# Optimization experiments

Measured on AMD Instinct MI355X. Metric: run time of the kernel, lower is better.

Reference implementation:

```python
import jax, jax.numpy as jnp
import numpy as np

# Topologies derived from init kwargs (inputs=64, outputs=64, state=512, net1 hidden=[512])
D = 64 + 64 + 512                      # 640 = concat(input, prev_output, state)
NET1 = [D, 512, 64]
NET3 = [D] + NET1 + [512]              # [640, 640, 512, 64, 512] (code reuses mutated net1 topo)
W_TOTAL = sum(NET3[j] * NET3[j + 1] for j in range(len(NET3) - 1))  # 802816
B_TOTAL = sum(NET3[1:])                # 1728
NET2 = [D] + NET1 + [W_TOTAL + B_TOTAL]  # [640, 640, 512, 64, 804544]


def _leaky(v):
    return jnp.where(v >= 0, v, 0.01 * v)


def setup_inputs() -> dict:
    key = jax.random.key(0)
    ks = jax.random.split(key, 16)
    inp = {
        "x": jax.random.normal(ks[0], (64,), jnp.float32),
        "prev_output": jnp.zeros((64,), jnp.float32),
        "state": jnp.zeros((512,), jnp.float32),
    }
    # net1 params (Linear stores W as [out, in])
    for i in range(len(NET1) - 1):
        inp[f"net1_w{i}"] = jax.random.normal(ks[1 + i], (NET1[i + 1], NET1[i]), jnp.float32) * 0.02
        inp[f"net1_b{i}"] = jnp.zeros((NET1[i + 1],), jnp.float32)
    # net2 params
    for i in range(len(NET2) - 1):
        inp[f"net2_w{i}"] = jax.random.normal(ks[5 + i], (NET2[i + 1], NET2[i]), jnp.float32) * 0.02
        inp[f"net2_b{i}"] = jnp.zeros((NET2[i + 1],), jnp.float32)
    return inp


def reference(x, prev_output, state,
              net1_w0, net1_b0, net1_w1, net1_b1,
              net2_w0, net2_b0, net2_w1, net2_b1,
              net2_w2, net2_b2, net2_w3, net2_b3):
    inpt = jnp.concatenate([x, prev_output, state])  # [640]

    # net2: hypernetwork producing flattened weights+biases for net3
    h = _leaky(net2_w0 @ inpt + net2_b0)
    h = _leaky(net2_w1 @ h + net2_b1)
    h = _leaky(net2_w2 @ h + net2_b2)
    x2 = jnp.tanh(net2_w3 @ h + net2_b3) * 0.5       # [W_TOTAL + B_TOTAL]
    weights = x2[:W_TOTAL]
    bias = x2[W_TOTAL:]

    # net3: apply generated weights sequentially (state update)
    x3 = inpt
    wi, bi = 0, 0
    for j in range(1, len(NET3)):
        out_d, in_d = NET3[j], NET3[j - 1]
        W = weights[wi:wi + out_d * in_d].reshape(out_d, in_d)
        b = bias[bi:bi + out_d]
        x3 = W @ x3 + b                               # 1D: x3 @ W.T == W @ x3
        if j != len(NET3) - 1:
            x3 = _leaky(x3)
        wi += out_d * in_d
        bi += out_d
    new_state = x3                                    # [512]

    # net1: output head
    h1 = _leaky(net1_w0 @ inpt + net1_b0)
    out = net1_w1 @ h1 + net1_b1                      # [64]

    # torch forward returns only `out`; new_state is the persistent buffer
    # update. We concatenate both so the full step math is observable.
    return jnp.concatenate([out, new_state])          # [576]
```

## Files before the change

kernel.cpp:

```cpp
#include <hip/hip_runtime.h>
#include <math.h>


#define WS_H0    0
#define WS_H1N1  640
#define WS_H1N2  1152
#define WS_H2    1664
#define WS_INPT  1728
#define WS_X3A   2368
#define WS_X3B   3008
#define WS_T     4096

#define N_ROWS   804544
#define N_WAVES  12571

typedef float vf4 __attribute__((ext_vector_type(4)));

__device__ __forceinline__ float leaky_f(float v) { return v >= 0.0f ? v : 0.01f * v; }

__device__ __forceinline__ float inpt_at(int i, const float* x, const float* po, const float* st) {
  return i < 64 ? x[i] : (i < 128 ? po[i - 64] : st[i - 128]);
}

__device__ __forceinline__ float half_tanh(float d) {
  float t = exp2f(d * 2.8853900817779268f);
  return 0.5f - __builtin_amdgcn_rcpf(t + 1.0f);
}

template <int IN>
__device__ __forceinline__ float row_dot(const float* __restrict__ wrow, const float* s_in, int lane) {
  const float4* w4 = (const float4*)wrow;
  const float4* s4 = (const float4*)s_in;
  float acc = 0.f;
  for (int j = lane; j < IN / 4; j += 64) {
    float4 a = w4[j];
    float4 b = s4[j];
    acc += a.x * b.x + a.y * b.y + a.z * b.z + a.w * b.w;
  }
  for (int off = 32; off; off >>= 1) acc += __shfl_xor(acc, off, 64);
  return acc;
}

__global__ __launch_bounds__(256) void k1a(const float* __restrict__ x, const float* __restrict__ po,
                                           const float* __restrict__ st,
                                           const float* __restrict__ w2_0, const float* __restrict__ b2_0,
                                           const float* __restrict__ w1_0, const float* __restrict__ b1_0,
                                           float* __restrict__ ws) {
  __shared__ __align__(16) float s_in[640];
  for (int i = threadIdx.x; i < 640; i += 256) {
    float v = inpt_at(i, x, po, st);
    s_in[i] = v;
    ws[WS_INPT + i] = v;
  }
  __syncthreads();
  int wave = threadIdx.x >> 6, lane = threadIdx.x & 63;
  int o = blockIdx.x * 4 + wave;
  const float* wrow;
  float bias;
  float* dst;
  if (o < 640) {
    wrow = w2_0 + (long long)o * 640; bias = b2_0[o]; dst = ws + WS_H0 + o;
  } else {
    int oo = o - 640;
    wrow = w1_0 + (long long)oo * 640; bias = b1_0[oo]; dst = ws + WS_H1N1 + oo;
  }
  float acc = row_dot<640>(wrow, s_in, lane);
  if (lane == 0) *dst = leaky_f(acc + bias);
}

__global__ __launch_bounds__(256) void k1b(const float* __restrict__ w2_1, const float* __restrict__ b2_1,
                                           const float* __restrict__ w1_1, const float* __restrict__ b1_1,
                                           float* __restrict__ ws, float* __restrict__ out) {
  __shared__ __align__(16) float s_h0[640];
  __shared__ __align__(16) float s_h1[512];
  for (int i = threadIdx.x; i < 640; i += 256) s_h0[i] = ws[WS_H0 + i];
  for (int i = threadIdx.x; i < 512; i += 256) s_h1[i] = ws[WS_H1N1 + i];
  __syncthreads();
  int wave = threadIdx.x >> 6, lane = threadIdx.x & 63;
  int o = blockIdx.x * 4 + wave;
  if (o < 512) {
    float acc = row_dot<640>(w2_1 + (long long)o * 640, s_h0, lane);
    if (lane == 0) ws[WS_H1N2 + o] = leaky_f(acc + b2_1[o]);
  } else {
    int oo = o - 512;
    float acc = row_dot<512>(w1_1 + (long long)oo * 512, s_h1, lane);
    if (lane == 0) out[oo] = acc + b1_1[oo];
  }
}

__global__ __launch_bounds__(256) void k1c(const float* __restrict__ w2_2, const float* __restrict__ b2_2,
                                           float* __restrict__ ws) {
  __shared__ __align__(16) float s_h[512];
  for (int i = threadIdx.x; i < 512; i += 256) s_h[i] = ws[WS_H1N2 + i];
  __syncthreads();
  int wave = threadIdx.x >> 6, lane = threadIdx.x & 63;
  int o = blockIdx.x * 4 + wave;
  float acc = row_dot<512>(w2_2 + (long long)o * 512, s_h, lane);
  if (lane == 0) ws[WS_H2 + o] = leaky_f(acc + b2_2[o]);
}

__global__ __launch_bounds__(256) void bigT(const float* __restrict__ w3, const float* __restrict__ b3,
                                            const float* __restrict__ h2p, float* __restrict__ t) {
  int wid = blockIdx.x * 4 + (threadIdx.x >> 6);
  if (wid >= N_WAVES) return;
  const int lane = threadIdx.x & 63;
  const int g = lane >> 4;
  const int gl = lane & 15;
  float4 hv = ((const float4*)h2p)[gl];
  const long long base = (long long)wid * 64;
  const vf4* wp = (const vf4*)(w3 + (base << 6));
  vf4 v[16];
#pragma unroll
  for (int q = 0; q < 16; q++) v[q] = __builtin_nontemporal_load(&wp[((q * 4 + g) << 4) + gl]);
#pragma unroll
  for (int q = 0; q < 16; q++) {
    float d = v[q].x * hv.x + v[q].y * hv.y + v[q].z * hv.z + v[q].w * hv.w;
    d += __shfl_xor(d, 1, 64);
    d += __shfl_xor(d, 2, 64);
    d += __shfl_xor(d, 4, 64);
    d += __shfl_xor(d, 8, 64);
    if (gl == 0) {
      long long r = base + q * 4 + g;
      t[r] = half_tanh(d + b3[r]);
    }
  }
}

template <int IN, bool LEAKY>
__global__ __launch_bounds__(256) void gml(const float* __restrict__ t, const float* __restrict__ x3in,
                                           float* __restrict__ x3out, long long wi, long long brow,
                                           int OUT) {
  __shared__ __align__(16) float s_in[IN];
  for (int i = threadIdx.x; i < IN; i += 256) s_in[i] = x3in[i];
  __syncthreads();
  int wave = threadIdx.x >> 6, lane = threadIdx.x & 63;
  int o = blockIdx.x * 4 + wave;
  if (o >= OUT) return;
  float acc = row_dot<IN>(t + wi + (long long)o * IN, s_in, lane);
  if (lane == 0) {
    acc += t[brow + o];
    x3out[o] = LEAKY ? leaky_f(acc) : acc;
  }
}

__global__ __launch_bounds__(1024) void gmlTail(const float* __restrict__ t, const float* __restrict__ ws,
                                                float* __restrict__ out) {
  __shared__ __align__(16) float s_b[512];
  __shared__ __align__(16) float s_c[64];
  const int tid = threadIdx.x;
  const int wave = tid >> 6, lane = tid & 63;
  for (int i = tid; i < 512; i += 1024) s_b[i] = ws[WS_X3B + i];
  __syncthreads();
#pragma unroll
  for (int r = 0; r < 4; r++) {
    int o = wave + r * 16;
    float acc = row_dot<512>(t + 737280 + (long long)o * 512, s_b, lane);
    if (lane == 0) s_c[o] = leaky_f(acc + t[803968 + o]);
  }
  __syncthreads();
  const int g = lane >> 4, gl = lane & 15;
  float4 xc4 = ((const float4*)s_c)[gl];
#pragma unroll
  for (int r = 0; r < 8; r++) {
    int o = r * 64 + wave * 4 + g;
    const float4* row = (const float4*)(t + 770048 + (long long)o * 64);
    float4 wv = row[gl];
    float a = wv.x * xc4.x + wv.y * xc4.y + wv.z * xc4.z + wv.w * xc4.w;
    a += __shfl_xor(a, 1, 64);
    a += __shfl_xor(a, 2, 64);
    a += __shfl_xor(a, 4, 64);
    a += __shfl_xor(a, 8, 64);
    if (gl == 0) out[64 + o] = a + t[804032 + o];
  }
}

extern "C" void kernel_launch(void* const* d_in, const int* in_sizes, int n_in,
                              void* d_out, int out_size, void* d_ws, size_t ws_size,
                              hipStream_t stream) {
  const float* x    = (const float*)d_in[0];
  const float* po   = (const float*)d_in[1];
  const float* st   = (const float*)d_in[2];
  const float* w1_0 = (const float*)d_in[3];
  const float* b1_0 = (const float*)d_in[4];
  const float* w1_1 = (const float*)d_in[5];
  const float* b1_1 = (const float*)d_in[6];
  const float* w2_0 = (const float*)d_in[7];
  const float* b2_0 = (const float*)d_in[8];
  const float* w2_1 = (const float*)d_in[9];
  const float* b2_1 = (const float*)d_in[10];
  const float* w2_2 = (const float*)d_in[11];
  const float* b2_2 = (const float*)d_in[12];
  const float* w3   = (const float*)d_in[13];
  const float* b3   = (const float*)d_in[14];
  float* ws  = (float*)d_ws;
  float* out = (float*)d_out;
  float* t   = ws + WS_T;

  k1a<<<288, 256, 0, stream>>>(x, po, st, w2_0, b2_0, w1_0, b1_0, ws);
  k1b<<<144, 256, 0, stream>>>(w2_1, b2_1, w1_1, b1_1, ws, out);
  k1c<<<16, 256, 0, stream>>>(w2_2, b2_2, ws);
  bigT<<<(N_WAVES + 3) / 4, 256, 0, stream>>>(w3, b3, ws + WS_H2, t);
  gml<640, true><<<160, 256, 0, stream>>>(t, ws + WS_INPT, ws + WS_X3A, 0LL, 802816LL, 640);
  gml<640, true><<<128, 256, 0, stream>>>(t, ws + WS_X3A, ws + WS_X3B, 409600LL, 803456LL, 512);
  gmlTail<<<1, 1024, 0, stream>>>(t, ws, out);
}
```

Baseline: 332.6 us.

## Fuse small layers via last-block atomic counters and coalesce bigT output stores

Merges the k1c layer into k1b and the second generated layer into the tail kernel. In each case the last block to finish, detected with an atomic counter and thread fences, runs the follow-on work, which removes two kernel launches and their inter-kernel gaps. bigT now gathers each row's dot product into one lane and writes one coalesced store per lane, and it drops the nontemporal loads. The trade-off is that the fused tail work runs serially on a single block, and the counters must be reset each call, which k1a does.

```diff
diff --git a/kernel.cpp b/kernel.cpp
--- a/kernel.cpp
+++ b/kernel.cpp
@@ -9,12 +9,12 @@
 #define WS_INPT  1728
 #define WS_X3A   2368
 #define WS_X3B   3008
+#define WS_CNT1  3584
+#define WS_CNT2  3585
 #define WS_T     4096
 
 #define N_ROWS   804544
 #define N_WAVES  12571
-
-typedef float vf4 __attribute__((ext_vector_type(4)));
 
 __device__ __forceinline__ float leaky_f(float v) { return v >= 0.0f ? v : 0.01f * v; }
 
@@ -46,6 +46,7 @@
                                            const float* __restrict__ w2_0, const float* __restrict__ b2_0,
                                            const float* __restrict__ w1_0, const float* __restrict__ b1_0,
                                            float* __restrict__ ws) {
+  if (blockIdx.x == 0 && threadIdx.x < 2) ((int*)ws)[WS_CNT1 + threadIdx.x] = 0;
   __shared__ __align__(16) float s_in[640];
   for (int i = threadIdx.x; i < 640; i += 256) {
     float v = inpt_at(i, x, po, st);
@@ -70,9 +71,11 @@
 
 __global__ __launch_bounds__(256) void k1b(const float* __restrict__ w2_1, const float* __restrict__ b2_1,
                                            const float* __restrict__ w1_1, const float* __restrict__ b1_1,
+                                           const float* __restrict__ w2_2, const float* __restrict__ b2_2,
                                            float* __restrict__ ws, float* __restrict__ out) {
   __shared__ __align__(16) float s_h0[640];
   __shared__ __align__(16) float s_h1[512];
+  __shared__ int s_last;
   for (int i = threadIdx.x; i < 640; i += 256) s_h0[i] = ws[WS_H0 + i];
   for (int i = threadIdx.x; i < 512; i += 256) s_h1[i] = ws[WS_H1N1 + i];
   __syncthreads();
@@ -86,17 +89,20 @@
     float acc = row_dot<512>(w1_1 + (long long)oo * 512, s_h1, lane);
     if (lane == 0) out[oo] = acc + b1_1[oo];
   }
-}
-
-__global__ __launch_bounds__(256) void k1c(const float* __restrict__ w2_2, const float* __restrict__ b2_2,
-                                           float* __restrict__ ws) {
-  __shared__ __align__(16) float s_h[512];
-  for (int i = threadIdx.x; i < 512; i += 256) s_h[i] = ws[WS_H1N2 + i];
-  __syncthreads();
-  int wave = threadIdx.x >> 6, lane = threadIdx.x & 63;
-  int o = blockIdx.x * 4 + wave;
-  float acc = row_dot<512>(w2_2 + (long long)o * 512, s_h, lane);
-  if (lane == 0) ws[WS_H2 + o] = leaky_f(acc + b2_2[o]);
+  __syncthreads();
+  __threadfence();
+  if (threadIdx.x == 0) s_last = (atomicAdd((int*)ws + WS_CNT1, 1) == (int)gridDim.x - 1);
+  __syncthreads();
+  if (!s_last) return;
+  __threadfence();
+  for (int i = threadIdx.x; i < 512; i += 256) s_h1[i] = ws[WS_H1N2 + i];
+  __syncthreads();
+#pragma unroll
+  for (int r = 0; r < 16; r++) {
+    int o2 = r * 4 + wave;
+    float acc = row_dot<512>(w2_2 + (long long)o2 * 512, s_h1, lane);
+    if (lane == 0) ws[WS_H2 + o2] = leaky_f(acc + b2_2[o2]);
+  }
 }
 
 __global__ __launch_bounds__(256) void bigT(const float* __restrict__ w3, const float* __restrict__ b3,
@@ -108,10 +114,13 @@
   const int gl = lane & 15;
   float4 hv = ((const float4*)h2p)[gl];
   const long long base = (long long)wid * 64;
-  const vf4* wp = (const vf4*)(w3 + (base << 6));
-  vf4 v[16];
-#pragma unroll
-  for (int q = 0; q < 16; q++) v[q] = __builtin_nontemporal_load(&wp[((q * 4 + g) << 4) + gl]);
+  const int myrow = (gl << 2) + g;
+  float bmine = b3[base + myrow];
+  const float4* wp = (const float4*)(w3 + (base << 6));
+  float4 v[16];
+#pragma unroll
+  for (int q = 0; q < 16; q++) v[q] = wp[((q * 4 + g) << 4) + gl];
+  float myd = 0.f;
 #pragma unroll
   for (int q = 0; q < 16; q++) {
     float d = v[q].x * hv.x + v[q].y * hv.y + v[q].z * hv.z + v[q].w * hv.w;
@@ -119,11 +128,9 @@
     d += __shfl_xor(d, 2, 64);
     d += __shfl_xor(d, 4, 64);
     d += __shfl_xor(d, 8, 64);
-    if (gl == 0) {
-      long long r = base + q * 4 + g;
-      t[r] = half_tanh(d + b3[r]);
-    }
-  }
+    if (gl == q) myd = d;
+  }
+  t[base + myrow] = half_tanh(myd + bmine);
 }
 
 template <int IN, bool LEAKY>
@@ -143,34 +150,48 @@
   }
 }
 
-__global__ __launch_bounds__(1024) void gmlTail(const float* __restrict__ t, const float* __restrict__ ws,
-                                                float* __restrict__ out) {
-  __shared__ __align__(16) float s_b[512];
+__global__ __launch_bounds__(1024) void gml2Tail(const float* __restrict__ t, float* __restrict__ ws,
+                                                 float* __restrict__ out) {
+  __shared__ __align__(16) float s_in[640];
   __shared__ __align__(16) float s_c[64];
+  __shared__ int s_last;
   const int tid = threadIdx.x;
   const int wave = tid >> 6, lane = tid & 63;
-  for (int i = tid; i < 512; i += 1024) s_b[i] = ws[WS_X3B + i];
+  for (int i = tid; i < 640; i += 1024) s_in[i] = ws[WS_X3A + i];
+  __syncthreads();
+  {
+    int o = blockIdx.x * 16 + wave;
+    float acc = row_dot<640>(t + 409600 + (long long)o * 640, s_in, lane);
+    if (lane == 0) ws[WS_X3B + o] = leaky_f(acc + t[803456 + o]);
+  }
+  __syncthreads();
+  __threadfence();
+  if (tid == 0) s_last = (atomicAdd((int*)ws + WS_CNT2, 1) == (int)gridDim.x - 1);
+  __syncthreads();
+  if (!s_last) return;
+  __threadfence();
+  for (int i = tid; i < 512; i += 1024) s_in[i] = ws[WS_X3B + i];
   __syncthreads();
 #pragma unroll
   for (int r = 0; r < 4; r++) {
-    int o = wave + r * 16;
-    float acc = row_dot<512>(t + 737280 + (long long)o * 512, s_b, lane);
-    if (lane == 0) s_c[o] = leaky_f(acc + t[803968 + o]);
-  }
-  __syncthreads();
-  const int g = lane >> 4, gl = lane & 15;
-  float4 xc4 = ((const float4*)s_c)[gl];
+    int o3 = wave + r * 16;
+    float acc = row_dot<512>(t + 737280 + (long long)o3 * 512, s_in, lane);
+    if (lane == 0) s_c[o3] = leaky_f(acc + t[803968 + o3]);
+  }
+  __syncthreads();
+  const int g = lane >> 4, glx = lane & 15;
+  float4 xc4 = ((const float4*)s_c)[glx];
 #pragma unroll
   for (int r = 0; r < 8; r++) {
-    int o = r * 64 + wave * 4 + g;
-    const float4* row = (const float4*)(t + 770048 + (long long)o * 64);
-    float4 wv = row[gl];
+    int o4 = r * 64 + wave * 4 + g;
+    const float4* row = (const float4*)(t + 770048 + (long long)o4 * 64);
+    float4 wv = row[glx];
     float a = wv.x * xc4.x + wv.y * xc4.y + wv.z * xc4.z + wv.w * xc4.w;
     a += __shfl_xor(a, 1, 64);
     a += __shfl_xor(a, 2, 64);
     a += __shfl_xor(a, 4, 64);
     a += __shfl_xor(a, 8, 64);
-    if (gl == 0) out[64 + o] = a + t[804032 + o];
+    if (glx == 0) out[64 + o4] = a + t[804032 + o4];
   }
 }
 
@@ -197,10 +218,8 @@
   float* t   = ws + WS_T;
 
   k1a<<<288, 256, 0, stream>>>(x, po, st, w2_0, b2_0, w1_0, b1_0, ws);
-  k1b<<<144, 256, 0, stream>>>(w2_1, b2_1, w1_1, b1_1, ws, out);
-  k1c<<<16, 256, 0, stream>>>(w2_2, b2_2, ws);
+  k1b<<<144, 256, 0, stream>>>(w2_1, b2_1, w1_1, b1_1, w2_2, b2_2, ws, out);
   bigT<<<(N_WAVES + 3) / 4, 256, 0, stream>>>(w3, b3, ws + WS_H2, t);
   gml<640, true><<<160, 256, 0, stream>>>(t, ws + WS_INPT, ws + WS_X3A, 0LL, 802816LL, 640);
-  gml<640, true><<<128, 256, 0, stream>>>(t, ws + WS_X3A, ws + WS_X3B, 409600LL, 803456LL, 512);
-  gmlTail<<<1, 1024, 0, stream>>>(t, ws, out);
-}
+  gml2Tail<<<32, 1024, 0, stream>>>(t, ws, out);
+}
```

Result: slower. 378.9 us (+13.9%).
